# Kernel tuning notes

Hardware: AMD Instinct MI355X
Metric: run time of the kernel (lower is better)

## Reference

```python
import jax, jax.numpy as jnp
import numpy as np

# ---- module hyperparameters (from init_kwargs) ----
KL_TEMP = 4.0
NUM_CLASSES = 100
POLICY_NUMS = 7          # linear out dim = POLICY_NUMS + 2 (identity, classes, policies)
FEATURE_NUMS = 128       # linear in dim = concat of two 64-d policy features
POS_W = (1.0, 0.5, 0.001)
NEG_W = (1.0, 0.5, 0.001)
KD_CE_W = (1.0, 1.0)
LOSS_W = (1.0, 1.0, 1.0)
BATCH = 2048


def setup_inputs() -> dict:
    key = jax.random.key(0)
    ks = jax.random.split(key, 9)
    O = POLICY_NUMS + 2
    return {
        "student_logits": jax.random.normal(ks[0], (BATCH, NUM_CLASSES), jnp.float32),
        "teacher_logits": jax.random.normal(ks[1], (BATCH, NUM_CLASSES), jnp.float32),
        "student_policy": jax.random.normal(ks[2], (BATCH, FEATURE_NUMS // 2), jnp.float32),
        "teacher_policy": jax.random.normal(ks[3], (BATCH, FEATURE_NUMS // 2), jnp.float32),
        "W1": jax.random.normal(ks[4], (O, FEATURE_NUMS), jnp.float32) * 0.08,  # frozen teacher linear
        "bias1": jax.random.normal(ks[5], (O,), jnp.float32) * 0.01,
        "W2": jax.random.normal(ks[6], (O, FEATURE_NUMS), jnp.float32) * 0.08,  # trainable student linear
        "bias2": jax.random.normal(ks[7], (O,), jnp.float32) * 0.01,
        "targets": jax.random.randint(ks[8], (BATCH, 1, POLICY_NUMS + 1), 0, 10, dtype=jnp.int32),
    }


def _kldiv_mean(inp, tgt):
    # torch KLDivLoss(reduction='mean'): mean over all elems of target*(log(target)-input), zero where target<=0
    safe = jnp.where(tgt > 0, tgt, 1.0)
    return jnp.where(tgt > 0, tgt * (jnp.log(safe) - inp), 0.0).mean()


def _wmean(loss, tgt, pw, nw):
    return jnp.where(tgt == 1.0, loss * pw, loss * nw).mean()


def _pair_linear(feat, W, bias):
    # L[i, j] = W @ concat(f_even[j], f_odd[i]) + bias, computed without materializing [b1,b1,2f]
    f = feat.shape[-1]
    f1, f2 = feat[0::2], feat[1::2]                       # [b1, f] each
    A = f1 @ W[:, :f].T                                   # [b1, O]  (j part)
    B = f2 @ W[:, f:].T                                   # [b1, O]  (i part)
    return B[:, None, :] + A[None, :, :] + bias           # [b1, b1, O]


def _policy_loss(teacher_policy, student_policy, targets, W1, bias1, W2, bias2):
    B = student_policy.shape[0]
    b1 = B // 2
    dt = student_policy.dtype

    Ls = _pair_linear(student_policy, W2, bias2)          # [b1,b1,O]
    Lt = jax.lax.stop_gradient(_pair_linear(teacher_policy, W1, bias1))

    sI, sC = Ls[..., 0], Ls[..., 1]
    sP = Ls[..., 2:].reshape(b1 * b1, POLICY_NUMS)
    tI, tC = Lt[..., 0], Lt[..., 1]
    tP = Lt[..., 2:].reshape(b1 * b1, POLICY_NUMS)

    eye = jnp.eye(b1, dtype=dt)
    # off-diagonal identity entries are detached for the student (teacher already no-grad)
    sI = eye * sI + (1.0 - eye) * jax.lax.stop_gradient(sI)

    t = targets.reshape(B, POLICY_NUMS + 1)
    t1, t2 = t[0::2], t[1::2]
    Teq = (t1[None, :, :] == t2[:, None, :]).astype(dt)   # [b1,b1,P+1]

    classes_value = 1.0 / (NUM_CLASSES - 1) + 1.0
    identity_value = 1.0 / (b1 - 1) + 1.0
    gC = Teq[..., 0] * classes_value - 1.0 / (NUM_CLASSES - 1)
    gP = Teq[..., 1:].reshape(b1 * b1, POLICY_NUMS) * 2.0 - 1.0
    gI = eye * identity_value - 1.0 / (b1 - 1)

    kl_loss = (_wmean((sI - tI) ** 2, gI, POS_W[0], NEG_W[0])
               + _wmean((sC - tC) ** 2, gC, POS_W[1], NEG_W[1])
               + _wmean((sP - tP) ** 2, gP, POS_W[2], NEG_W[2]))

    # KLDivLoss(reduction='mean') returns a scalar; torch.where broadcasts it, so .mean() of weights scales it
    ce_loss = (_kldiv_mean(sI, gI) * jnp.where(gI == 1.0, POS_W[0], NEG_W[0]).mean()
               + _kldiv_mean(sC, gC) * jnp.where(gC == 1.0, POS_W[1], NEG_W[1]).mean()
               + _wmean((sP - gP) ** 2, gP, POS_W[2], NEG_W[2]))

    return KD_CE_W[0] * kl_loss + KD_CE_W[1] * ce_loss


def reference(student_logits, teacher_logits, student_policy, teacher_policy, W1, bias1, W2, bias2, targets):
    B = student_logits.shape[0]
    # ---- CE loss (targets last dim <= 15 -> integer class label at column 0) ----
    labels = targets.reshape(B, -1)[:, 0]
    logp = jax.nn.log_softmax(student_logits, axis=1)
    ce_loss = -jnp.take_along_axis(logp, labels[:, None], axis=1).mean()

    # ---- KD KL loss (KLDivLoss reduction='mean' over all elements) ----
    t_prob = jax.nn.softmax(teacher_logits / KL_TEMP, axis=1)
    s_logp = jax.nn.log_softmax(student_logits / KL_TEMP, axis=1)
    kl_loss = _kldiv_mean(s_logp, t_prob) * (KL_TEMP ** 2)

    # ---- pairwise policy loss (the fusion-heavy path) ----
    policy_loss = _policy_loss(teacher_policy, student_policy, targets, W1, bias1, W2, bias2)

    return LOSS_W[0] * ce_loss + LOSS_W[1] * kl_loss + LOSS_W[2] * policy_loss
```

## Files before the change

kernel.cpp:

```cpp
#include <hip/hip_runtime.h>
#include <math.h>

#define NCLS   100
#define BATCH_ 2048
#define OK     9
#define FHALF  64

#define NLOGB  128
#define NPOLB  16
#define NBLK   (NLOGB + NPOLB)

#define LP_OFF 0
#define PS_OFF (LP_OFF + NLOGB * 2)
#define PB_OFF (PS_OFF + NPOLB * 72)

__device__ int g_arrive = 0;

__device__ __forceinline__ float waveSum(float v) {
#pragma unroll
    for (int off = 32; off; off >>= 1) v += __shfl_xor(v, off, 64);
    return v;
}
__device__ __forceinline__ float waveMax(float v) {
#pragma unroll
    for (int off = 32; off; off >>= 1) v = fmaxf(v, __shfl_xor(v, off, 64));
    return v;
}

__global__ __launch_bounds__(1024) void fused_kernel(
        const float* __restrict__ slog, const float* __restrict__ tlog,
        const float* __restrict__ spol, const float* __restrict__ tpol,
        const float* __restrict__ W1,   const float* __restrict__ W2,
        const int*   __restrict__ tgt,
        const float* __restrict__ bias1, const float* __restrict__ bias2,
        float* __restrict__ ws, float* __restrict__ out)
{
    __shared__ float4 w1s4[OK * 32];
    __shared__ float4 w2s4[OK * 32];
    __shared__ float bkt[320];
    __shared__ float redL[32];
    __shared__ float statsC[72];
    __shared__ float bktC[320];
    __shared__ float cekl[8];
    __shared__ int   lastFlag;

    const int tid  = threadIdx.x;
    const int wave = tid >> 6;
    const int lane = tid & 63;

    if (blockIdx.x < NLOGB) {
        const int r = blockIdx.x * 16 + wave;
        const float* x = slog + r * NCLS;
        const float* y = tlog + r * NCLS;
        const int label = tgt[r * 8];
        const bool has2 = lane < (NCLS - 64);
        float x1 = x[lane];
        float y1 = y[lane];
        float x2 = has2 ? x[lane + 64] : -3.0e38f;
        float y2 = has2 ? y[lane + 64] : -3.0e38f;
        float xl = x[label];
        float mx = waveMax(fmaxf(x1, x2));
        float my = waveMax(fmaxf(y1, y2));
        float se1  = waveSum(expf(x1 - mx) + (has2 ? expf(x2 - mx) : 0.f));
        float se4s = waveSum(expf((x1 - mx) * 0.25f) + (has2 ? expf((x2 - mx) * 0.25f) : 0.f));
        float e1 = expf((y1 - my) * 0.25f);
        float e2 = has2 ? expf((y2 - my) * 0.25f) : 0.f;
        float se4t = waveSum(e1 + e2);
        float tnum = waveSum(e1 * (y1 - x1) * 0.25f + (has2 ? e2 * (y2 - x2) * 0.25f : 0.f));
        if (lane == 0) {
            float logZ1  = mx + logf(se1);
            float logZ4s = mx * 0.25f + logf(se4s);
            float logZ4t = my * 0.25f + logf(se4t);
            redL[wave * 2]     = logZ1 - xl;
            redL[wave * 2 + 1] = tnum / se4t + logZ4s - logZ4t;
        }
        __syncthreads();
        if (tid < 2) {
            float s = 0.f;
#pragma unroll
            for (int w = 0; w < 16; ++w) s += redL[w * 2 + tid];
            ws[LP_OFF + blockIdx.x * 2 + tid] = s;
        }
    } else {
        const int pb = blockIdx.x - NLOGB;
        if (tid < OK * 32) {
            w1s4[tid] = ((const float4*)W1)[tid];
            w2s4[tid] = ((const float4*)W2)[tid];
        }
        if (tid < 320) bkt[tid] = 0.f;
        __syncthreads();

        float As[OK], Bs[OK];
        if (tid < 64) {
            const int i = pb * 64 + tid;
            const float4* f1s = (const float4*)(spol + (2 * i) * FHALF);
            const float4* f2s = (const float4*)(spol + (2 * i + 1) * FHALF);
            const float4* f1t = (const float4*)(tpol + (2 * i) * FHALF);
            const float4* f2t = (const float4*)(tpol + (2 * i + 1) * FHALF);

            float At[OK], Bt[OK];
#pragma unroll
            for (int k = 0; k < OK; ++k) { As[k] = 0.f; Bs[k] = 0.f; At[k] = 0.f; Bt[k] = 0.f; }
            for (int f4 = 0; f4 < FHALF / 4; ++f4) {
                float4 a4 = f1s[f4], b4 = f2s[f4], c4 = f1t[f4], d4 = f2t[f4];
#pragma unroll
                for (int k = 0; k < OK; ++k) {
                    const float4 wa2 = w2s4[k * 32 + f4];
                    const float4 wb2 = w2s4[k * 32 + 16 + f4];
                    const float4 wa1 = w1s4[k * 32 + f4];
                    const float4 wb1 = w1s4[k * 32 + 16 + f4];
                    As[k] = fmaf(a4.x, wa2.x, As[k]);
                    As[k] = fmaf(a4.y, wa2.y, As[k]);
                    As[k] = fmaf(a4.z, wa2.z, As[k]);
                    As[k] = fmaf(a4.w, wa2.w, As[k]);
                    Bs[k] = fmaf(b4.x, wb2.x, Bs[k]);
                    Bs[k] = fmaf(b4.y, wb2.y, Bs[k]);
                    Bs[k] = fmaf(b4.z, wb2.z, Bs[k]);
                    Bs[k] = fmaf(b4.w, wb2.w, Bs[k]);
                    At[k] = fmaf(c4.x, wa1.x, At[k]);
                    At[k] = fmaf(c4.y, wa1.y, At[k]);
                    At[k] = fmaf(c4.z, wa1.z, At[k]);
                    At[k] = fmaf(c4.w, wa1.w, At[k]);
                    Bt[k] = fmaf(d4.x, wb1.x, Bt[k]);
                    Bt[k] = fmaf(d4.y, wb1.y, Bt[k]);
                    Bt[k] = fmaf(d4.z, wb1.z, Bt[k]);
                    Bt[k] = fmaf(d4.w, wb1.w, Bt[k]);
                }
            }

#pragma unroll
            for (int k = 0; k < OK; ++k) {
                float du = Bs[k] - Bt[k], dw = As[k] - At[k];
                float v0 = waveSum(du),     v1 = waveSum(du * du);
                float v2 = waveSum(dw),     v3 = waveSum(dw * dw);
                float v4 = waveSum(Bs[k]),  v5 = waveSum(Bs[k] * Bs[k]);
                float v6 = waveSum(As[k]),  v7 = waveSum(As[k] * As[k]);
                if (lane == 0) {
                    float* p = ws + PS_OFF + pb * 72 + k * 8;
                    p[0] = v0; p[1] = v1; p[2] = v2; p[3] = v3;
                    p[4] = v4; p[5] = v5; p[6] = v6; p[7] = v7;
                }
            }

            const int* t1r = tgt + (2 * i) * 8;
            const int* t2r = tgt + (2 * i + 1) * 8;
#pragma unroll
            for (int c0 = 0; c0 < 8; ++c0) {
                int v1i = t1r[c0], v2i = t2r[c0];
                atomicAdd(&bkt[0 * 80 + c0 * 10 + v1i], 1.0f);
                atomicAdd(&bkt[1 * 80 + c0 * 10 + v2i], 1.0f);
                atomicAdd(&bkt[2 * 80 + c0 * 10 + v1i], As[c0 + 1]);
                atomicAdd(&bkt[3 * 80 + c0 * 10 + v2i], Bs[c0 + 1]);
            }
        }
        __syncthreads();
        if (tid < 320) ws[PB_OFF + pb * 320 + tid] = bkt[tid];
    }

    __syncthreads();
    if (tid == 0) {
        __threadfence();
        int old = atomicAdd(&g_arrive, 1);
        int last = (old == NBLK - 1);
        if (last) {
            g_arrive = 0;
            __threadfence();
        }
        lastFlag = last;
    }
    __syncthreads();
    if (!lastFlag) return;

    float ce = 0.f, kl = 0.f;
    if (tid < NLOGB) {
        ce = ws[LP_OFF + tid * 2];
        kl = ws[LP_OFF + tid * 2 + 1];
    }
    ce = waveSum(ce); kl = waveSum(kl);
    if (lane == 0 && wave < 2) { cekl[wave * 2] = ce; cekl[wave * 2 + 1] = kl; }

    if (tid < 72) {
        float s = 0.f;
#pragma unroll
        for (int b = 0; b < NPOLB; ++b) s += ws[PS_OFF + b * 72 + tid];
        statsC[tid] = s;
    }
    if (tid < 320) {
        float s = 0.f;
#pragma unroll
        for (int b = 0; b < NPOLB; ++b) s += ws[PB_OFF + b * 320 + tid];
        bktC[tid] = s;
    }
    __syncthreads();

    if (tid == 0) {
        const double N = 1024.0, M = 1048576.0;
        double ce_main = (double)(cekl[0] + cekl[2]) / (double)BATCH_;
        double kl_main = (double)(cekl[1] + cekl[3]) * 16.0
                       / (double)(BATCH_ * NCLS);

        double kl_pol = 0.0, Sp_acc = 0.0;
        double SumL[OK], SumL2[OK];
        for (int k = 0; k < OK; ++k) {
            const float* p = &statsC[k * 8];
            double D1u = p[0], D2u = p[1], D1w = p[2], D2w = p[3];
            double U1 = p[4], U2 = p[5], Wa1 = p[6], Wa2 = p[7];
            double cd = (double)bias2[k] - (double)bias1[k];
            double b  = (double)bias2[k];
            double S = N * D2u + N * (D2w + 2.0 * cd * D1w + N * cd * cd)
                     + 2.0 * D1u * (D1w + N * cd);
            if (k == 0)      kl_pol += S / M;
            else if (k == 1) kl_pol += 0.5 * S / M;
            else             Sp_acc += S;
            SumL[k]  = N * U1 + N * Wa1 + M * b;
            SumL2[k] = N * U2 + N * (Wa2 + 2.0 * b * Wa1 + N * b * b)
                     + 2.0 * U1 * (Wa1 + N * b);
        }
        kl_pol += 0.001 * Sp_acc / (7.0 * M);

        double ce_I = -((double)statsC[4] + (double)statsC[6] + N * (double)bias2[0]) / M;

        const float* cnt1 = &bktC[0];
        const float* cnt2 = &bktC[80];
        const float* sA   = &bktC[160];
        const float* sB   = &bktC[240];
        double ce_C = 0.0, ceP = 0.0;
        for (int c0 = 0; c0 < 8; ++c0) {
            double ms = 0.0, pc = 0.0;
            for (int v = 0; v < 10; ++v) {
                double c1 = (double)cnt1[c0 * 10 + v], c2 = (double)cnt2[c0 * 10 + v];
                ms += c1 * (double)sB[c0 * 10 + v] + c2 * (double)sA[c0 * 10 + v];
                pc += c1 * c2;
            }
            ms += (double)bias2[c0 + 1] * pc;
            if (c0 == 0) {
                ce_C = -0.5 * ms / M;
            } else {
                int k = c0 + 1;
                double sg = 2.0 * ms - SumL[k];
                ceP += SumL2[k] - 2.0 * sg + M;
            }
        }
        ceP *= 0.001 / (7.0 * M);

        out[0] = (float)(ce_main + kl_main + kl_pol + ce_I + ce_C + ceP);
    }
}

extern "C" void kernel_launch(void* const* d_in, const int* in_sizes, int n_in,
                              void* d_out, int out_size, void* d_ws, size_t ws_size,
                              hipStream_t stream) {
    const float* slog = (const float*)d_in[0];
    const float* tlog = (const float*)d_in[1];
    const float* spol = (const float*)d_in[2];
    const float* tpol = (const float*)d_in[3];
    const float* W1   = (const float*)d_in[4];
    const float* b1   = (const float*)d_in[5];
    const float* W2   = (const float*)d_in[6];
    const float* b2   = (const float*)d_in[7];
    const int*   tgt  = (const int*)d_in[8];
    float* ws = (float*)d_ws;

    fused_kernel<<<NBLK, 1024, 0, stream>>>(slog, tlog, spol, tpol, W1, W2, tgt,
                                            b1, b2, ws, (float*)d_out);
}
```

Baseline: 95.42 us.

## Split policy matvecs across four waves and parallelize reductions per output

```diff
diff --git a/kernel.cpp b/kernel.cpp
--- a/kernel.cpp
+++ b/kernel.cpp
@@ -37,8 +37,9 @@
 {
     __shared__ float4 w1s4[OK * 32];
     __shared__ float4 w2s4[OK * 32];
-    __shared__ float bkt[320];
-    __shared__ float redL[32];
+    __shared__ float  res[4 * OK * 64];
+    __shared__ float  bkt[320];
+    __shared__ float  redL[32];
     __shared__ float statsC[72];
     __shared__ float bktC[320];
     __shared__ float cekl[8];
@@ -90,67 +91,64 @@
         if (tid < 320) bkt[tid] = 0.f;
         __syncthreads();
 
-        float As[OK], Bs[OK];
-        if (tid < 64) {
-            const int i = pb * 64 + tid;
-            const float4* f1s = (const float4*)(spol + (2 * i) * FHALF);
-            const float4* f2s = (const float4*)(spol + (2 * i + 1) * FHALF);
-            const float4* f1t = (const float4*)(tpol + (2 * i) * FHALF);
-            const float4* f2t = (const float4*)(tpol + (2 * i + 1) * FHALF);
-
-            float At[OK], Bt[OK];
-#pragma unroll
-            for (int k = 0; k < OK; ++k) { As[k] = 0.f; Bs[k] = 0.f; At[k] = 0.f; Bt[k] = 0.f; }
+        if (wave < 4) {
+            const int i = pb * 64 + lane;
+            const float* fbase = (wave & 2) ? tpol : spol;
+            const float4* feat = (const float4*)(fbase + (2 * i + (wave & 1)) * FHALF);
+            const float4* wb   = (wave & 2) ? w1s4 : w2s4;
+            const int colOff   = (wave & 1) ? 16 : 0;
+
+            float acc[OK];
+#pragma unroll
+            for (int k = 0; k < OK; ++k) acc[k] = 0.f;
             for (int f4 = 0; f4 < FHALF / 4; ++f4) {
-                float4 a4 = f1s[f4], b4 = f2s[f4], c4 = f1t[f4], d4 = f2t[f4];
+                float4 fv = feat[f4];
 #pragma unroll
                 for (int k = 0; k < OK; ++k) {
-                    const float4 wa2 = w2s4[k * 32 + f4];
-                    const float4 wb2 = w2s4[k * 32 + 16 + f4];
-                    const float4 wa1 = w1s4[k * 32 + f4];
-                    const float4 wb1 = w1s4[k * 32 + 16 + f4];
-                    As[k] = fmaf(a4.x, wa2.x, As[k]);
-                    As[k] = fmaf(a4.y, wa2.y, As[k]);
-                    As[k] = fmaf(a4.z, wa2.z, As[k]);
-                    As[k] = fmaf(a4.w, wa2.w, As[k]);
-                    Bs[k] = fmaf(b4.x, wb2.x, Bs[k]);
-                    Bs[k] = fmaf(b4.y, wb2.y, Bs[k]);
-                    Bs[k] = fmaf(b4.z, wb2.z, Bs[k]);
-                    Bs[k] = fmaf(b4.w, wb2.w, Bs[k]);
-                    At[k] = fmaf(c4.x, wa1.x, At[k]);
-                    At[k] = fmaf(c4.y, wa1.y, At[k]);
-                    At[k] = fmaf(c4.z, wa1.z, At[k]);
-                    At[k] = fmaf(c4.w, wa1.w, At[k]);
-                    Bt[k] = fmaf(d4.x, wb1.x, Bt[k]);
-                    Bt[k] = fmaf(d4.y, wb1.y, Bt[k]);
-                    Bt[k] = fmaf(d4.z, wb1.z, Bt[k]);
-                    Bt[k] = fmaf(d4.w, wb1.w, Bt[k]);
+                    const float4 wv = wb[k * 32 + colOff + f4];
+                    acc[k] = fmaf(fv.x, wv.x, acc[k]);
+                    acc[k] = fmaf(fv.y, wv.y, acc[k]);
+                    acc[k] = fmaf(fv.z, wv.z, acc[k]);
+                    acc[k] = fmaf(fv.w, wv.w, acc[k]);
                 }
             }
-
-#pragma unroll
-            for (int k = 0; k < OK; ++k) {
-                float du = Bs[k] - Bt[k], dw = As[k] - At[k];
-                float v0 = waveSum(du),     v1 = waveSum(du * du);
-                float v2 = waveSum(dw),     v3 = waveSum(dw * dw);
-                float v4 = waveSum(Bs[k]),  v5 = waveSum(Bs[k] * Bs[k]);
-                float v6 = waveSum(As[k]),  v7 = waveSum(As[k] * As[k]);
-                if (lane == 0) {
-                    float* p = ws + PS_OFF + pb * 72 + k * 8;
-                    p[0] = v0; p[1] = v1; p[2] = v2; p[3] = v3;
-                    p[4] = v4; p[5] = v5; p[6] = v6; p[7] = v7;
-                }
-            }
-
-            const int* t1r = tgt + (2 * i) * 8;
-            const int* t2r = tgt + (2 * i + 1) * 8;
+#pragma unroll
+            for (int k = 0; k < OK; ++k)
+                res[(wave * OK + k) * 64 + lane] = acc[k];
+        }
+        __syncthreads();
+
+        if (wave < OK) {
+            const int k = wave;
+            float A = res[(0 * OK + k) * 64 + lane];
+            float B = res[(1 * OK + k) * 64 + lane];
+            float C = res[(2 * OK + k) * 64 + lane];
+            float D = res[(3 * OK + k) * 64 + lane];
+            float du = B - D, dw = A - C;
+            float v0 = waveSum(du),  v1 = waveSum(du * du);
+            float v2 = waveSum(dw),  v3 = waveSum(dw * dw);
+            float v4 = waveSum(B),   v5 = waveSum(B * B);
+            float v6 = waveSum(A),   v7 = waveSum(A * A);
+            if (lane == 0) {
+                float* p = ws + PS_OFF + pb * 72 + k * 8;
+                p[0] = v0; p[1] = v1; p[2] = v2; p[3] = v3;
+                p[4] = v4; p[5] = v5; p[6] = v6; p[7] = v7;
+            }
+        }
+        if (wave == 9) {
+            const int i = pb * 64 + lane;
+            const int4* t1q = (const int4*)(tgt + (2 * i) * 8);
+            const int4* t2q = (const int4*)(tgt + (2 * i + 1) * 8);
+            int4 t1a = t1q[0], t1b = t1q[1];
+            int4 t2a = t2q[0], t2b = t2q[1];
+            int t1[8] = { t1a.x, t1a.y, t1a.z, t1a.w, t1b.x, t1b.y, t1b.z, t1b.w };
+            int t2[8] = { t2a.x, t2a.y, t2a.z, t2a.w, t2b.x, t2b.y, t2b.z, t2b.w };
 #pragma unroll
             for (int c0 = 0; c0 < 8; ++c0) {
-                int v1i = t1r[c0], v2i = t2r[c0];
-                atomicAdd(&bkt[0 * 80 + c0 * 10 + v1i], 1.0f);
-                atomicAdd(&bkt[1 * 80 + c0 * 10 + v2i], 1.0f);
-                atomicAdd(&bkt[2 * 80 + c0 * 10 + v1i], As[c0 + 1]);
-                atomicAdd(&bkt[3 * 80 + c0 * 10 + v2i], Bs[c0 + 1]);
+                atomicAdd(&bkt[0 * 80 + c0 * 10 + t1[c0]], 1.0f);
+                atomicAdd(&bkt[1 * 80 + c0 * 10 + t2[c0]], 1.0f);
+                atomicAdd(&bkt[2 * 80 + c0 * 10 + t1[c0]], res[(0 * OK + c0 + 1) * 64 + lane]);
+                atomicAdd(&bkt[3 * 80 + c0 * 10 + t2[c0]], res[(1 * OK + c0 + 1) * 64 + lane]);
             }
         }
         __syncthreads();
```

New measurement: 87.82 us. -8.0%, faster.
